# Performance work log

Measured on AMD Instinct MI355X. Metric: run time of the kernel, lower is better.

Reference implementation:

```python
import jax, jax.numpy as jnp
import numpy as np

D_IN, D_K, D_V = 1024, 1024, 1024
B, S = 4, 2048

def setup_inputs() -> dict:
    key = jax.random.key(0)
    ks = jax.random.split(key, 7)
    s = 1.0 / np.sqrt(D_IN)
    return {
        "x": jax.random.normal(ks[0], (B, S, D_IN), dtype=jnp.float32),
        "Wq": jax.random.uniform(ks[1], (D_IN, D_K), jnp.float32, -s, s),
        "bq": jax.random.uniform(ks[2], (D_K,), jnp.float32, -s, s),
        "Wk": jax.random.uniform(ks[3], (D_IN, D_K), jnp.float32, -s, s),
        "bk": jax.random.uniform(ks[4], (D_K,), jnp.float32, -s, s),
        "Wv": jax.random.uniform(ks[5], (D_IN, D_V), jnp.float32, -s, s),
        "bv": jax.random.uniform(ks[6], (D_V,), jnp.float32, -s, s),
    }

def reference(x, Wq, bq, Wk, bk, Wv, bv):
    # QKV projections: [B,S,d_in] @ [d_in,d] + b
    Q = x @ Wq + bq  # [B,S,d_k]
    K = x @ Wk + bk  # [B,S,d_k]
    V = x @ Wv + bv  # [B,S,d_v]
    # Non-standard recipe: softmax over UNSCALED scores, then divide output by sqrt(d_k)
    scores = jnp.einsum('bqd,bkd->bqk', Q, K)  # [B,S,S]
    attn = jax.nn.softmax(scores, axis=2)
    out = jnp.einsum('bqk,bkv->bqv', attn, V) / jnp.sqrt(jnp.asarray(K.shape[2], dtype=x.dtype))
    return out
```

## Files before the change

kernel.cpp:

```cpp
#include <hip/hip_runtime.h>
#include <stdint.h>

typedef unsigned short u16;
typedef _Float16 f16;
typedef _Float16 f16x8 __attribute__((ext_vector_type(8)));
typedef float f32x4 __attribute__((ext_vector_type(4)));

#define DIN 1024
#define SEQ 2048
#define NB 4
#define MB (1u << 20)


__device__ __forceinline__ void gload_lds16(const void* g, void* l) {
    __builtin_amdgcn_global_load_lds(
        (__attribute__((address_space(1))) void*)(uintptr_t)g,
        (__attribute__((address_space(3))) void*)l,
        16, 0, 0);
}

__device__ __forceinline__ int xcd_swz(int h, int cpx) {
    return (h & 7) * cpx + (h >> 3);
}


__device__ __forceinline__ void gemm_tile(
    const char* __restrict__ A, const char* __restrict__ B,
    int lda, int ldb, int ksteps, char* smem, f32x4 acc[4][4])
{
    const int lane = threadIdx.x & 63;
    const int wave = threadIdx.x >> 6;

    #pragma unroll
    for (int m = 0; m < 4; ++m)
        #pragma unroll
        for (int n = 0; n < 4; ++n)
            acc[m][n] = (f32x4){0.f, 0.f, 0.f, 0.f};

    const char* ga[4];
    const char* gb[4];
    int ldsoff[4];
    #pragma unroll
    for (int i = 0; i < 4; ++i) {
        int La = (wave * 4 + i) * 1024 + lane * 16;
        int r  = La >> 7;
        int cb = La & 127;
        int sc = cb ^ ((r & 7) << 4);
        ga[i] = A + (size_t)r * (size_t)(lda * 2) + sc;
        gb[i] = B + (size_t)r * (size_t)(ldb * 2) + sc;
        ldsoff[i] = (wave * 4 + i) * 1024;
    }

    const int wr = (wave >> 1) * 64;
    const int wc = (wave & 1) * 64;

    for (int ks = 0; ks < ksteps; ++ks) {
        #pragma unroll
        for (int i = 0; i < 4; ++i) {
            gload_lds16(ga[i], smem + ldsoff[i]);
            gload_lds16(gb[i], smem + 16384 + ldsoff[i]);
            ga[i] += 128;
            gb[i] += 128;
        }
        __syncthreads();

        #pragma unroll
        for (int kk = 0; kk < 2; ++kk) {
            const int kb = kk * 64 + ((lane >> 4) << 4);
            f16x8 af[4], bfv[4];
            #pragma unroll
            for (int m = 0; m < 4; ++m) {
                int r = wr + m * 16 + (lane & 15);
                af[m] = *(const f16x8*)(smem + r * 128 + (kb ^ ((r & 7) << 4)));
            }
            #pragma unroll
            for (int n = 0; n < 4; ++n) {
                int r = wc + n * 16 + (lane & 15);
                bfv[n] = *(const f16x8*)(smem + 16384 + r * 128 + (kb ^ ((r & 7) << 4)));
            }
            #pragma unroll
            for (int m = 0; m < 4; ++m)
                #pragma unroll
                for (int n = 0; n < 4; ++n)
                    acc[m][n] = __builtin_amdgcn_mfma_f32_16x16x32_f16(
                        af[m], bfv[n], acc[m][n], 0, 0, 0);
        }
        __syncthreads();
    }
}


__global__ __launch_bounds__(256) void k_prep(
    const float* __restrict__ x, f16* __restrict__ xh,
    const float* __restrict__ Wq, const float* __restrict__ Wk,
    const float* __restrict__ Wv, f16* __restrict__ wt)
{
    __shared__ float tile[32][33];
    const int bid = blockIdx.x;
    if (bid < 2048) {
        const int n8 = (NB * SEQ * DIN) / 8;
        for (int idx = bid * 256 + threadIdx.x; idx < n8; idx += 2048 * 256) {
            f32x4 a = ((const f32x4*)x)[(size_t)idx * 2];
            f32x4 b = ((const f32x4*)x)[(size_t)idx * 2 + 1];
            f16x8 o;
            o[0] = (f16)a[0]; o[1] = (f16)a[1]; o[2] = (f16)a[2]; o[3] = (f16)a[3];
            o[4] = (f16)b[0]; o[5] = (f16)b[1]; o[6] = (f16)b[2]; o[7] = (f16)b[3];
            ((f16x8*)xh)[idx] = o;
        }
    } else {
        const int wb = bid - 2048;
        const int mtx = wb >> 10;
        const int rem = wb & 1023;
        const int n0 = (rem & 31) * 32, k0 = (rem >> 5) * 32;
        const float* W = (mtx == 0) ? Wq : (mtx == 1 ? Wk : Wv);
        const int c = threadIdx.x & 31, r0 = threadIdx.x >> 5;
        #pragma unroll
        for (int rr = r0; rr < 32; rr += 8)
            tile[rr][c] = W[(size_t)(k0 + rr) * DIN + n0 + c];
        __syncthreads();
        f16* o = wt + (size_t)mtx * DIN * DIN;
        #pragma unroll
        for (int rr = r0; rr < 32; rr += 8)
            o[(size_t)(n0 + rr) * DIN + k0 + c] = (f16)tile[c][rr];
    }
}

__global__ __launch_bounds__(256) void k_gemm_qkv(
    const f16* __restrict__ xh, const f16* __restrict__ wt,
    const float* __restrict__ bq, const float* __restrict__ bk,
    const float* __restrict__ bv,
    f16* __restrict__ Q, f16* __restrict__ K, f16* __restrict__ Vt)
{
    __shared__ __align__(16) char smem[32768];
    f32x4 acc[4][4];
    const int sid = xcd_swz(blockIdx.x, 192);
    const int blkN = sid % 24;
    const int blkM = sid / 24;
    gemm_tile((const char*)(xh + (size_t)blkM * 128 * DIN),
              (const char*)(wt + (size_t)blkN * 128 * DIN),
              DIN, DIN, DIN / 64, smem, acc);

    const int lane = threadIdx.x & 63;
    const int wave = threadIdx.x >> 6;
    const int row0 = blkM * 128 + (wave >> 1) * 64;
    const int col0 = blkN * 128 + (wave & 1) * 64;

    if (col0 >= 2048) {
        const int bb = row0 >> 11;
        const int sb = row0 & (SEQ - 1);
        f16* Vtb = Vt + (size_t)bb * DIN * SEQ;
        #pragma unroll
        for (int n = 0; n < 4; ++n) {
            int d = (col0 - 2048) + n * 16 + (lane & 15);
            float bias = bv[d];
            #pragma unroll
            for (int m = 0; m < 4; ++m) {
                #pragma unroll
                for (int j = 0; j < 4; ++j) {
                    int s = sb + m * 16 + (lane >> 4) * 4 + j;
                    Vtb[(size_t)d * SEQ + s] = (f16)(acc[m][n][j] + bias);
                }
            }
        }
    } else {
        f16* dst = (col0 < 1024) ? Q : K;
        const float* bsrc = (col0 < 1024) ? bq : bk;
        const int ncb = col0 & 1023;
        #pragma unroll
        for (int n = 0; n < 4; ++n) {
            int nc = ncb + n * 16 + (lane & 15);
            float bias = bsrc[nc];
            #pragma unroll
            for (int m = 0; m < 4; ++m) {
                #pragma unroll
                for (int j = 0; j < 4; ++j) {
                    int row = row0 + m * 16 + (lane >> 4) * 4 + j;
                    dst[(size_t)row * 1024 + nc] = (f16)(acc[m][n][j] + bias);
                }
            }
        }
    }
}

__global__ __launch_bounds__(256) void k_gemm_scores(
    const f16* __restrict__ Q, const f16* __restrict__ K, float* __restrict__ S)
{
    __shared__ __align__(16) char smem[32768];
    f32x4 acc[4][4];
    const int sid = xcd_swz(blockIdx.x, 128);
    const int bx = sid & 15;
    const int by = (sid >> 4) & 15;
    const int b  = sid >> 8;
    const f16* Qb = Q + (size_t)b * SEQ * 1024;
    const f16* Kb = K + (size_t)b * SEQ * 1024;
    gemm_tile((const char*)(Qb + (size_t)by * 128 * 1024),
              (const char*)(Kb + (size_t)bx * 128 * 1024),
              1024, 1024, 1024 / 64, smem, acc);

    float* Sb = S + (size_t)b * SEQ * SEQ;
    const int lane = threadIdx.x & 63;
    const int wave = threadIdx.x >> 6;
    const int row0 = by * 128 + (wave >> 1) * 64;
    const int col0 = bx * 128 + (wave & 1) * 64;
    #pragma unroll
    for (int m = 0; m < 4; ++m)
        #pragma unroll
        for (int n = 0; n < 4; ++n) {
            int col = col0 + n * 16 + (lane & 15);
            #pragma unroll
            for (int j = 0; j < 4; ++j) {
                int row = row0 + m * 16 + (lane >> 4) * 4 + j;
                Sb[(size_t)row * SEQ + col] = acc[m][n][j];
            }
        }
}

__global__ __launch_bounds__(256) void k_softmax(
    const float* __restrict__ S, f16* __restrict__ P)
{
    const size_t row = blockIdx.x;
    const float* s = S + row * SEQ;
    f16* p = P + row * SEQ;
    const int t = threadIdx.x;

    f32x4 x0 = ((const f32x4*)s)[t * 2];
    f32x4 x1 = ((const f32x4*)s)[t * 2 + 1];
    float v[8] = {x0[0], x0[1], x0[2], x0[3], x1[0], x1[1], x1[2], x1[3]};

    float mx = v[0];
    #pragma unroll
    for (int j = 1; j < 8; ++j) mx = fmaxf(mx, v[j]);
    #pragma unroll
    for (int o = 32; o; o >>= 1) mx = fmaxf(mx, __shfl_xor(mx, o, 64));
    __shared__ float red[8];
    if ((t & 63) == 0) red[t >> 6] = mx;
    __syncthreads();
    mx = fmaxf(fmaxf(red[0], red[1]), fmaxf(red[2], red[3]));

    float sum = 0.f;
    #pragma unroll
    for (int j = 0; j < 8; ++j) { v[j] = __expf(v[j] - mx); sum += v[j]; }
    #pragma unroll
    for (int o = 32; o; o >>= 1) sum += __shfl_xor(sum, o, 64);
    if ((t & 63) == 0) red[4 + (t >> 6)] = sum;
    __syncthreads();
    sum = (red[4] + red[5]) + (red[6] + red[7]);
    float inv = 1.0f / sum;

    f16x8 o8;
    #pragma unroll
    for (int j = 0; j < 8; ++j) o8[j] = (f16)(v[j] * inv);
    ((f16x8*)p)[t] = o8;
}

__global__ __launch_bounds__(256) void k_gemm_pv(
    const f16* __restrict__ P, const f16* __restrict__ Vt, float* __restrict__ out)
{
    __shared__ __align__(16) char smem[32768];
    f32x4 acc[4][4];
    const int sid = xcd_swz(blockIdx.x, 64);
    const int bx = sid & 7;
    const int by = (sid >> 3) & 15;
    const int b  = sid >> 7;
    const f16* Pb  = P  + (size_t)b * SEQ * SEQ;
    const f16* Vtb = Vt + (size_t)b * 1024 * SEQ;
    gemm_tile((const char*)(Pb  + (size_t)by * 128 * SEQ),
              (const char*)(Vtb + (size_t)bx * 128 * SEQ),
              SEQ, SEQ, SEQ / 64, smem, acc);

    float* ob = out + (size_t)b * SEQ * 1024;
    const int lane = threadIdx.x & 63;
    const int wave = threadIdx.x >> 6;
    const int row0 = by * 128 + (wave >> 1) * 64;
    const int col0 = bx * 128 + (wave & 1) * 64;
    #pragma unroll
    for (int m = 0; m < 4; ++m)
        #pragma unroll
        for (int n = 0; n < 4; ++n) {
            int col = col0 + n * 16 + (lane & 15);
            #pragma unroll
            for (int j = 0; j < 4; ++j) {
                int row = row0 + m * 16 + (lane >> 4) * 4 + j;
                ob[(size_t)row * 1024 + col] = acc[m][n][j] * 0.03125f;
            }
        }
}


extern "C" void kernel_launch(void* const* d_in, const int* in_sizes, int n_in,
                              void* d_out, int out_size, void* d_ws, size_t ws_size,
                              hipStream_t stream) {
    const float* x  = (const float*)d_in[0];
    const float* Wq = (const float*)d_in[1];
    const float* bq = (const float*)d_in[2];
    const float* Wk = (const float*)d_in[3];
    const float* bk = (const float*)d_in[4];
    const float* Wv = (const float*)d_in[5];
    const float* bv = (const float*)d_in[6];
    float* out = (float*)d_out;
    char* ws = (char*)d_ws;

    f16*  Q  = (f16*)(ws);
    f16*  K  = (f16*)(ws + (size_t)16 * MB);
    f16*  Vt = (f16*)(ws + (size_t)32 * MB);
    f16*  xh = (f16*)(ws + (size_t)48 * MB);
    f16*  wt = (f16*)(ws + (size_t)64 * MB);
    float* S = (float*)(ws + (size_t)48 * MB);
    f16*  P  = Q;

    const size_t needed = (size_t)112 * MB;
    if (ws_size < needed) return;

    k_prep<<<5120, 256, 0, stream>>>(x, xh, Wq, Wk, Wv, wt);
    k_gemm_qkv<<<1536, 256, 0, stream>>>(xh, wt, bq, bk, bv, Q, K, Vt);
    k_gemm_scores<<<1024, 256, 0, stream>>>(Q, K, S);
    k_softmax<<<NB * SEQ, 256, 0, stream>>>(S, P);
    k_gemm_pv<<<512, 256, 0, stream>>>(P, Vt, out);
}
```

Baseline: 173.5 us.

## Use 256x256 tile, 8-wave pipelined GEMM for QKV and score kernels

Replaces the 128x128 four-wave GEMM tile with a 256x256 eight-wave tile that double-buffers 128 KB of LDS, uses XOR-swizzled layouts and explicit barrier/waitcnt interleaving of MFMA with global-to-LDS loads. This raises arithmetic intensity per block and overlaps loads with compute, cutting global traffic for the QKV projection and the QK^T score GEMM. In exchange, the grid is much smaller (384 and 256 blocks), register pressure rises, and the 128 KB dynamic LDS with launch bounds of 2 blocks per CU may not actually fit two blocks per CU.

```diff
diff --git a/kernel.cpp b/kernel.cpp
--- a/kernel.cpp
+++ b/kernel.cpp
@@ -21,6 +21,115 @@
 
 __device__ __forceinline__ int xcd_swz(int h, int cpx) {
     return (h & 7) * cpx + (h >> 3);
+}
+
+__device__ __forceinline__ void barrier_raw() {
+    asm volatile("" ::: "memory");
+    __builtin_amdgcn_s_barrier();
+    asm volatile("" ::: "memory");
+}
+__device__ __forceinline__ void lgkm0() {
+    asm volatile("s_waitcnt lgkmcnt(0)" ::: "memory");
+    __builtin_amdgcn_sched_barrier(0);
+}
+template<int N>
+__device__ __forceinline__ void wait_vm() {
+    asm volatile("s_waitcnt vmcnt(%0)" :: "i"(N) : "memory");
+}
+
+
+__device__ __forceinline__ void gemm256(
+    const char* __restrict__ A, const char* __restrict__ B,
+    int ldab, int ldbb, int nt, char* smem, f32x4 acc[8][4])
+{
+    const int tid  = threadIdx.x;
+    const int lane = tid & 63;
+    const int wave = tid >> 6;
+    const int ln15 = lane & 15;
+    const int k16  = (lane >> 4) << 4;
+    const int wmB  = (wave >> 2) * 128;
+    const int wnB  = (wave & 3) * 64;
+
+    #pragma unroll
+    for (int m = 0; m < 8; ++m)
+        #pragma unroll
+        for (int n = 0; n < 4; ++n)
+            acc[m][n] = (f32x4){0.f, 0.f, 0.f, 0.f};
+
+    const char* pA[2];
+    const char* pB[2];
+    #pragma unroll
+    for (int i = 0; i < 2; ++i) {
+        const int La = i * 8192 + tid * 16;
+        const int r  = La >> 7;
+        const int sc = (La & 127) ^ ((r & 7) << 4);
+        pA[i] = A + (size_t)r * ldab + sc;
+        pB[i] = B + (size_t)r * ldbb + sc;
+    }
+    const int ldsw = wave * 1024;
+
+    f16x8 a[4][2], b[4][2];
+
+    auto stage = [&](int g) {
+        if (g < 4 * nt) {
+            const int ks  = g >> 2;
+            const int isB = ((g & 2) == 0);
+            const int h   = g & 1;
+            char* l = smem + (ks & 1) * 65536 + (isB ? 32768 : 0) + h * 16384 + ldsw;
+            #pragma unroll
+            for (int i = 0; i < 2; ++i) {
+                const char* gp = (isB ? pB[i] + (size_t)(h * 128) * ldbb
+                                      : pA[i] + (size_t)(h * 128) * ldab) + ks * 128;
+                gload_lds16(gp, l + i * 8192);
+            }
+        }
+    };
+
+#define RDA(qm) { _Pragma("unroll") for (int mf = 0; mf < 4; ++mf) { \
+        const int r = wmB + ((qm) * 4 + mf) * 16 + ln15; \
+        const int sw = (r & 7) << 4; \
+        const char* p = sAc + r * 128; \
+        a[mf][0] = *(const f16x8*)(p + ((k16) ^ sw)); \
+        a[mf][1] = *(const f16x8*)(p + ((64 + k16) ^ sw)); } }
+
+#define RDB() { _Pragma("unroll") for (int nf = 0; nf < 4; ++nf) { \
+        const int r = wnB + nf * 16 + ln15; \
+        const int sw = (r & 7) << 4; \
+        const char* p = sBc + r * 128; \
+        b[nf][0] = *(const f16x8*)(p + ((k16) ^ sw)); \
+        b[nf][1] = *(const f16x8*)(p + ((64 + k16) ^ sw)); } }
+
+#define MM(qm, nf0) { __builtin_amdgcn_s_setprio(1); \
+        _Pragma("unroll") for (int mf = 0; mf < 4; ++mf) \
+        _Pragma("unroll") for (int nf = (nf0); nf < (nf0) + 2; ++nf) { \
+            acc[(qm)*4+mf][nf] = __builtin_amdgcn_mfma_f32_16x16x32_f16( \
+                a[mf][0], b[nf][0], acc[(qm)*4+mf][nf], 0, 0, 0); \
+            acc[(qm)*4+mf][nf] = __builtin_amdgcn_mfma_f32_16x16x32_f16( \
+                a[mf][1], b[nf][1], acc[(qm)*4+mf][nf], 0, 0, 0); } \
+        __builtin_amdgcn_s_setprio(0); }
+
+    #pragma unroll
+    for (int g = 0; g < 8; ++g) stage(g);
+    wait_vm<8>();
+    barrier_raw();
+
+    for (int t = 0; t < nt; ++t) {
+        const char* sAc = smem + (t & 1) * 65536;
+        const char* sBc = sAc + 32768;
+        const int gb = 4 * (t + 2);
+        RDA(0); RDB();
+        barrier_raw(); lgkm0(); MM(0, 0); barrier_raw();
+        stage(gb + 0);
+        barrier_raw(); MM(0, 2); barrier_raw();
+        RDA(1); stage(gb + 1);
+        barrier_raw(); lgkm0(); MM(1, 0); barrier_raw();
+        stage(gb + 2); stage(gb + 3);
+        if (t < nt - 2) { wait_vm<8>(); } else if (t == nt - 2) { wait_vm<0>(); }
+        barrier_raw(); MM(1, 2); barrier_raw();
+    }
+#undef RDA
+#undef RDB
+#undef MM
 }
 
 
@@ -125,25 +234,25 @@
     }
 }
 
-__global__ __launch_bounds__(256) void k_gemm_qkv(
+__global__ __launch_bounds__(512, 2) void k_gemm_qkv8(
     const f16* __restrict__ xh, const f16* __restrict__ wt,
     const float* __restrict__ bq, const float* __restrict__ bk,
     const float* __restrict__ bv,
     f16* __restrict__ Q, f16* __restrict__ K, f16* __restrict__ Vt)
 {
-    __shared__ __align__(16) char smem[32768];
-    f32x4 acc[4][4];
-    const int sid = xcd_swz(blockIdx.x, 192);
-    const int blkN = sid % 24;
-    const int blkM = sid / 24;
-    gemm_tile((const char*)(xh + (size_t)blkM * 128 * DIN),
-              (const char*)(wt + (size_t)blkN * 128 * DIN),
-              DIN, DIN, DIN / 64, smem, acc);
+    extern __shared__ char smem[];
+    f32x4 acc[8][4];
+    const int sid = xcd_swz(blockIdx.x, 48);
+    const int blkN = sid % 12;
+    const int blkM = sid / 12;
+    gemm256((const char*)(xh + (size_t)blkM * 256 * DIN),
+            (const char*)(wt + (size_t)blkN * 256 * DIN),
+            DIN * 2, DIN * 2, DIN / 64, smem, acc);
 
     const int lane = threadIdx.x & 63;
     const int wave = threadIdx.x >> 6;
-    const int row0 = blkM * 128 + (wave >> 1) * 64;
-    const int col0 = blkN * 128 + (wave & 1) * 64;
+    const int row0 = blkM * 256 + (wave >> 2) * 128;
+    const int col0 = blkN * 256 + (wave & 3) * 64;
 
     if (col0 >= 2048) {
         const int bb = row0 >> 11;
@@ -154,7 +263,7 @@
             int d = (col0 - 2048) + n * 16 + (lane & 15);
             float bias = bv[d];
             #pragma unroll
-            for (int m = 0; m < 4; ++m) {
+            for (int m = 0; m < 8; ++m) {
                 #pragma unroll
                 for (int j = 0; j < 4; ++j) {
                     int s = sb + m * 16 + (lane >> 4) * 4 + j;
@@ -171,7 +280,7 @@
             int nc = ncb + n * 16 + (lane & 15);
             float bias = bsrc[nc];
             #pragma unroll
-            for (int m = 0; m < 4; ++m) {
+            for (int m = 0; m < 8; ++m) {
                 #pragma unroll
                 for (int j = 0; j < 4; ++j) {
                     int row = row0 + m * 16 + (lane >> 4) * 4 + j;
@@ -182,28 +291,26 @@
     }
 }
 
-__global__ __launch_bounds__(256) void k_gemm_scores(
+__global__ __launch_bounds__(512, 2) void k_gemm_scores8(
     const f16* __restrict__ Q, const f16* __restrict__ K, float* __restrict__ S)
 {
-    __shared__ __align__(16) char smem[32768];
-    f32x4 acc[4][4];
-    const int sid = xcd_swz(blockIdx.x, 128);
-    const int bx = sid & 15;
-    const int by = (sid >> 4) & 15;
-    const int b  = sid >> 8;
-    const f16* Qb = Q + (size_t)b * SEQ * 1024;
-    const f16* Kb = K + (size_t)b * SEQ * 1024;
-    gemm_tile((const char*)(Qb + (size_t)by * 128 * 1024),
-              (const char*)(Kb + (size_t)bx * 128 * 1024),
-              1024, 1024, 1024 / 64, smem, acc);
+    extern __shared__ char smem[];
+    f32x4 acc[8][4];
+    const int sid = xcd_swz(blockIdx.x, 32);
+    const int bx = sid & 7, by = (sid >> 3) & 7, b = sid >> 6;
+    const f16* Qb = Q + (size_t)b * SEQ * DIN;
+    const f16* Kb = K + (size_t)b * SEQ * DIN;
+    gemm256((const char*)(Qb + (size_t)by * 256 * DIN),
+            (const char*)(Kb + (size_t)bx * 256 * DIN),
+            DIN * 2, DIN * 2, DIN / 64, smem, acc);
 
     float* Sb = S + (size_t)b * SEQ * SEQ;
     const int lane = threadIdx.x & 63;
     const int wave = threadIdx.x >> 6;
-    const int row0 = by * 128 + (wave >> 1) * 64;
-    const int col0 = bx * 128 + (wave & 1) * 64;
-    #pragma unroll
-    for (int m = 0; m < 4; ++m)
+    const int row0 = by * 256 + (wave >> 2) * 128;
+    const int col0 = bx * 256 + (wave & 3) * 64;
+    #pragma unroll
+    for (int m = 0; m < 8; ++m)
         #pragma unroll
         for (int n = 0; n < 4; ++n) {
             int col = col0 + n * 16 + (lane & 15);
@@ -311,9 +418,14 @@
     const size_t needed = (size_t)112 * MB;
     if (ws_size < needed) return;
 
+    hipFuncSetAttribute((const void*)k_gemm_qkv8,
+                        hipFuncAttributeMaxDynamicSharedMemorySize, 131072);
+    hipFuncSetAttribute((const void*)k_gemm_scores8,
+                        hipFuncAttributeMaxDynamicSharedMemorySize, 131072);
+
     k_prep<<<5120, 256, 0, stream>>>(x, xh, Wq, Wk, Wv, wt);
-    k_gemm_qkv<<<1536, 256, 0, stream>>>(xh, wt, bq, bk, bv, Q, K, Vt);
-    k_gemm_scores<<<1024, 256, 0, stream>>>(Q, K, S);
+    k_gemm_qkv8<<<384, 512, 131072, stream>>>(xh, wt, bq, bk, bv, Q, K, Vt);
+    k_gemm_scores8<<<256, 512, 131072, stream>>>(Q, K, S);
     k_softmax<<<NB * SEQ, 256, 0, stream>>>(S, P);
     k_gemm_pv<<<512, 256, 0, stream>>>(P, Vt, out);
 }
```

After: 177.7 us (median of 4 runs). 1.02x slower.
